# Kernel optimization log

Measured on AMD Instinct MI355X. Metric: run time of the kernel, lower is better.

The kernel has to match this reference:

```python
import jax, jax.numpy as jnp
import numpy as np
from jax import lax


def setup_inputs() -> dict:
    key = jax.random.key(0)
    k1, k2 = jax.random.split(key)
    C, H, W = 64, 224, 224
    C_out, hf, wf = 128, 3, 3
    x = jax.random.normal(k1, (C, H, W), dtype=jnp.float32)
    kernels = jax.random.normal(k2, (C_out, C, hf, wf), dtype=jnp.float32)
    return {"x": x, "kernels": kernels}


def reference(x, kernels):
    # Original builds im2col columns per output pixel then does k_col @ x_col,
    # i.e. a cross-correlation with 'valid' padding and stride 1.
    # lax.conv_general_dilated computes exactly this (no kernel flip).
    stride = 1
    out = lax.conv_general_dilated(
        x[None],                       # (1, C, H, W) NCHW
        kernels,                       # (C_out, C_in, hf, wf) OIHW
        window_strides=(stride, stride),
        padding="VALID",
        dimension_numbers=("NCHW", "OIHW", "NCHW"),
    )
    return out[0]                      # (C_out, H_out, W_out)
```

## Files before the change

### kernel.cpp

```cpp
#include <hip/hip_runtime.h>
#include <hip/hip_bf16.h>


#define H_IN   224
#define W_IN   224
#define C_OUT  128
#define H_OUT  222
#define W_OUT  222
#define XP     226
#define CPAD   72
#define TW     68

typedef __attribute__((ext_vector_type(8)))  short bf16x8;
typedef __attribute__((ext_vector_type(16))) float f32x16;

static __device__ __forceinline__ unsigned short f2bs(float f) {
    union { __hip_bfloat16 h; unsigned short u; } cv;
    cv.h = __float2bfloat16(f);
    return cv.u;
}

__global__ __launch_bounds__(256)
void transform_w_kernel(const float* __restrict__ w, __hip_bfloat16* __restrict__ wt)
{
    int idx = blockIdx.x * 256 + threadIdx.x;
    if (idx < 9 * 128 * 64) {
        int ij  = idx >> 13;
        int rem = idx & 8191;
        int co  = rem >> 6;
        int c   = rem & 63;
        wt[idx] = __float2bfloat16(w[(co * 64 + c) * 9 + ij]);
    }
}

__global__ __launch_bounds__(256)
void transpose_x_kernel(const float* __restrict__ x, __hip_bfloat16* __restrict__ xt)
{
    __shared__ __align__(16) unsigned short tile[64 * TW];
    const int h  = blockIdx.y;
    const int w0 = blockIdx.x * 64;
    const int t  = threadIdx.x;

    {
        const int wq = (t & 15) * 4;
        const int c0 = t >> 4;
        #pragma unroll
        for (int p = 0; p < 4; ++p) {
            const int c  = c0 + p * 16;
            const int wg = w0 + wq;
            float4 v = make_float4(0.f, 0.f, 0.f, 0.f);
            if (h < H_IN && wg < W_IN)
                v = *(const float4*)(x + ((size_t)c * H_IN + h) * W_IN + wg);
            ushort4 b;
            b.x = f2bs(v.x); b.y = f2bs(v.y); b.z = f2bs(v.z); b.w = f2bs(v.w);
            *(ushort4*)(tile + c * TW + wq) = b;
        }
    }
    __syncthreads();

    {
        const int wl = t >> 2;
        const int cq = (t & 3) * 16;
        const int wg = w0 + wl;
        if (wg < XP) {
            alignas(16) unsigned short r[16];
            #pragma unroll
            for (int k = 0; k < 16; ++k)
                r[k] = tile[(cq + k) * TW + wl];
            float4* d = (float4*)((unsigned short*)xt + ((size_t)h * XP + wg) * 64 + cq);
            d[0] = ((const float4*)r)[0];
            d[1] = ((const float4*)r)[1];
        }
    }
}

__global__ __launch_bounds__(256)
void conv_mfma_kernel(const __hip_bfloat16* __restrict__ xt,
                      const __hip_bfloat16* __restrict__ wt,
                      float* __restrict__ out)
{
    __shared__ __hip_bfloat16 xs[10 * 34 * CPAD];
    const int ow0 = blockIdx.x * 32;
    const int oh0 = blockIdx.y * 8;
    const int co0 = blockIdx.z * 64;
    const int tid = threadIdx.x;

    for (int q = tid; q < 10 * 34 * 8; q += 256) {
        int sub = q & 7;
        int pix = q >> 3;
        int row = pix / 34;
        int wc  = pix - row * 34;
        *(float4*)(xs + (row * 34 + wc) * CPAD + sub * 8) =
            *(const float4*)(xt + ((oh0 + row) * XP + (ow0 + wc)) * 64 + sub * 8);
    }
    __syncthreads();

    const int wave = tid >> 6;
    const int lane = tid & 63;
    const int n    = lane & 31;
    const int h    = lane >> 5;

    f32x16 acc[2][2] = {};

    #pragma unroll
    for (int i = 0; i < 3; ++i) {
        bf16x8 afr[3][2][4];
        #pragma unroll
        for (int jj = 0; jj < 3; ++jj)
            #pragma unroll
            for (int mi = 0; mi < 2; ++mi)
                #pragma unroll
                for (int t = 0; t < 4; ++t)
                    afr[jj][mi][t] = *(const bf16x8*)(wt +
                        ((i * 3 + jj) * 128 + co0 + mi * 32 + n) * 64 + t * 16 + h * 8);

        #pragma unroll
        for (int jj = 0; jj < 3; ++jj) {
            #pragma unroll
            for (int t = 0; t < 4; ++t) {
                bf16x8 bfr[2];
                #pragma unroll
                for (int ni = 0; ni < 2; ++ni)
                    bfr[ni] = *(const bf16x8*)(xs +
                        ((wave * 2 + ni + i) * 34 + n + jj) * CPAD + t * 16 + h * 8);
                #pragma unroll
                for (int mi = 0; mi < 2; ++mi)
                    #pragma unroll
                    for (int ni = 0; ni < 2; ++ni)
                        acc[mi][ni] = __builtin_amdgcn_mfma_f32_32x32x16_bf16(
                            afr[jj][mi][t], bfr[ni], acc[mi][ni], 0, 0, 0);
            }
        }
    }

    #pragma unroll
    for (int mi = 0; mi < 2; ++mi) {
        #pragma unroll
        for (int ni = 0; ni < 2; ++ni) {
            const int oh = oh0 + wave * 2 + ni;
            const int ow = ow0 + n;
            if (oh < H_OUT && ow < W_OUT) {
                #pragma unroll
                for (int r = 0; r < 16; ++r) {
                    int co = co0 + mi * 32 + (r & 3) + 8 * (r >> 2) + 4 * h;
                    out[(size_t)co * (H_OUT * W_OUT) + oh * W_OUT + ow] = acc[mi][ni][r];
                }
            }
        }
    }
}

extern "C" void kernel_launch(void* const* d_in, const int* in_sizes, int n_in,
                              void* d_out, int out_size, void* d_ws, size_t ws_size,
                              hipStream_t stream)
{
    const float* x = (const float*)d_in[0];
    const float* w = (const float*)d_in[1];
    float* out     = (float*)d_out;

    __hip_bfloat16* xt = (__hip_bfloat16*)d_ws;
    __hip_bfloat16* wt = (__hip_bfloat16*)((char*)d_ws + (size_t)XP * XP * 64 * 2);

    transform_w_kernel<<<288, 256, 0, stream>>>(w, wt);
    transpose_x_kernel<<<dim3(4, XP), 256, 0, stream>>>(x, xt);
    conv_mfma_kernel<<<dim3(7, 28, 2), 256, 0, stream>>>(xt, wt, out);
}
```

Measured before the change: 98.14 us.

## Stage weights through double-buffered LDS with a blocked weight layout

```diff
diff --git a/kernel.cpp b/kernel.cpp
--- a/kernel.cpp
+++ b/kernel.cpp
@@ -29,7 +29,8 @@
         int rem = idx & 8191;
         int co  = rem >> 6;
         int c   = rem & 63;
-        wt[idx] = __float2bfloat16(w[(co * 64 + c) * 9 + ij]);
+        wt[((ij * 8 + (c >> 3)) * 128 + co) * 8 + (c & 7)] =
+            __float2bfloat16(w[(co * 64 + c) * 9 + ij]);
     }
 }
 
@@ -80,6 +81,7 @@
                       float* __restrict__ out)
 {
     __shared__ __hip_bfloat16 xs[10 * 34 * CPAD];
+    __shared__ __hip_bfloat16 wsb[2][8 * 64 * 8];
     const int ow0 = blockIdx.x * 32;
     const int oh0 = blockIdx.y * 8;
     const int co0 = blockIdx.z * 64;
@@ -93,51 +95,77 @@
         *(float4*)(xs + (row * 34 + wc) * CPAD + sub * 8) =
             *(const float4*)(xt + ((oh0 + row) * XP + (ow0 + wc)) * 64 + sub * 8);
     }
+    {
+        const float4* s = (const float4*)(wt + (size_t)co0 * 8);
+        #pragma unroll
+        for (int k = 0; k < 2; ++k) {
+            int q  = k * 256 + tid;
+            int ks = q >> 6;
+            int cc = q & 63;
+            *(float4*)(&wsb[0][(ks * 64 + cc) * 8]) =
+                *(const float4*)(wt + ((0 * 8 + ks) * 128 + co0 + cc) * 8);
+        }
+        (void)s;
+    }
     __syncthreads();
 
     const int wave = tid >> 6;
     const int lane = tid & 63;
     const int n    = lane & 31;
     const int h    = lane >> 5;
+    const int r0   = wave * 2;
 
     f32x16 acc[2][2] = {};
 
     #pragma unroll
-    for (int i = 0; i < 3; ++i) {
-        bf16x8 afr[3][2][4];
+    for (int p = 0; p < 9; ++p) {
+        const int i  = p / 3;
+        const int jj = p - i * 3;
+        const int cb = p & 1;
+
+        float4 pf[2];
+        int ks0 = 0, cc0 = 0, ks1 = 0, cc1 = 0;
+        if (p < 8) {
+            #pragma unroll
+            for (int k = 0; k < 2; ++k) {
+                int q  = k * 256 + tid;
+                int ks = q >> 6;
+                int cc = q & 63;
+                pf[k] = *(const float4*)(wt + (((p + 1) * 8 + ks) * 128 + co0 + cc) * 8);
+                if (k == 0) { ks0 = ks; cc0 = cc; } else { ks1 = ks; cc1 = cc; }
+            }
+        }
+
         #pragma unroll
-        for (int jj = 0; jj < 3; ++jj)
+        for (int t = 0; t < 4; ++t) {
+            bf16x8 afr[2], bfr[2];
+            #pragma unroll
+            for (int mi = 0; mi < 2; ++mi)
+                afr[mi] = *(const bf16x8*)(&wsb[cb][((t * 2 + h) * 64 + mi * 32 + n) * 8]);
+            #pragma unroll
+            for (int ni = 0; ni < 2; ++ni)
+                bfr[ni] = *(const bf16x8*)(xs +
+                    ((i + r0 + ni) * 34 + n + jj) * CPAD + t * 16 + h * 8);
             #pragma unroll
             for (int mi = 0; mi < 2; ++mi)
                 #pragma unroll
-                for (int t = 0; t < 4; ++t)
-                    afr[jj][mi][t] = *(const bf16x8*)(wt +
-                        ((i * 3 + jj) * 128 + co0 + mi * 32 + n) * 64 + t * 16 + h * 8);
+                for (int ni = 0; ni < 2; ++ni)
+                    acc[mi][ni] = __builtin_amdgcn_mfma_f32_32x32x16_bf16(
+                        afr[mi], bfr[ni], acc[mi][ni], 0, 0, 0);
+        }
 
-        #pragma unroll
-        for (int jj = 0; jj < 3; ++jj) {
-            #pragma unroll
-            for (int t = 0; t < 4; ++t) {
-                bf16x8 bfr[2];
-                #pragma unroll
-                for (int ni = 0; ni < 2; ++ni)
-                    bfr[ni] = *(const bf16x8*)(xs +
-                        ((wave * 2 + ni + i) * 34 + n + jj) * CPAD + t * 16 + h * 8);
-                #pragma unroll
-                for (int mi = 0; mi < 2; ++mi)
-                    #pragma unroll
-                    for (int ni = 0; ni < 2; ++ni)
-                        acc[mi][ni] = __builtin_amdgcn_mfma_f32_32x32x16_bf16(
-                            afr[jj][mi][t], bfr[ni], acc[mi][ni], 0, 0, 0);
-            }
+        if (p < 8) {
+            *(float4*)(&wsb[1 - cb][(ks0 * 64 + cc0) * 8]) = pf[0];
+            *(float4*)(&wsb[1 - cb][(ks1 * 64 + cc1) * 8]) = pf[1];
         }
+        __syncthreads();
     }
 
     #pragma unroll
     for (int mi = 0; mi < 2; ++mi) {
         #pragma unroll
         for (int ni = 0; ni < 2; ++ni) {
-            const int oh = oh0 + wave * 2 + ni;
+            const int oh = oh0 + r0 + ni;
             const int ow = ow0 + n;
             if (oh < H_OUT && ow < W_OUT) {
                 #pragma unroll
```

New measurement: 88.08 us. 10.3% less time.

## Swizzle LDS input tile and reorder weight layout for coalesced fragment loads

Applied to the files above, without the earlier changes.

```diff
diff --git a/kernel.cpp b/kernel.cpp
--- a/kernel.cpp
+++ b/kernel.cpp
@@ -8,7 +8,6 @@
 #define H_OUT  222
 #define W_OUT  222
 #define XP     226
-#define CPAD   72
 #define TW     68
 
 typedef __attribute__((ext_vector_type(8)))  short bf16x8;
@@ -29,7 +28,8 @@
         int rem = idx & 8191;
         int co  = rem >> 6;
         int c   = rem & 63;
-        wt[idx] = __float2bfloat16(w[(co * 64 + c) * 9 + ij]);
+        wt[((ij * 8 + (c >> 3)) * 128 + co) * 8 + (c & 7)] =
+            __float2bfloat16(w[(co * 64 + c) * 9 + ij]);
     }
 }
 
@@ -79,7 +79,7 @@
                       const __hip_bfloat16* __restrict__ wt,
                       float* __restrict__ out)
 {
-    __shared__ __hip_bfloat16 xs[10 * 34 * CPAD];
+    __shared__ __hip_bfloat16 xs[10 * 34 * 64];
     const int ow0 = blockIdx.x * 32;
     const int oh0 = blockIdx.y * 8;
     const int co0 = blockIdx.z * 64;
@@ -90,7 +90,8 @@
         int pix = q >> 3;
         int row = pix / 34;
         int wc  = pix - row * 34;
-        *(float4*)(xs + (row * 34 + wc) * CPAD + sub * 8) =
+        int chunk = sub ^ (wc & 3);
+        *(float4*)(xs + pix * 64 + chunk * 8) =
             *(const float4*)(xt + ((oh0 + row) * XP + (ow0 + wc)) * 64 + sub * 8);
     }
     __syncthreads();
@@ -99,37 +100,39 @@
     const int lane = tid & 63;
     const int n    = lane & 31;
     const int h    = lane >> 5;
+    const int r0   = wave * 2;
 
     f32x16 acc[2][2] = {};
 
     #pragma unroll
-    for (int i = 0; i < 3; ++i) {
-        bf16x8 afr[3][2][4];
+    for (int p = 0; p < 9; ++p) {
+        const int i  = p / 3;
+        const int jj = p - i * 3;
+
+        bf16x8 afr[4][2];
         #pragma unroll
-        for (int jj = 0; jj < 3; ++jj)
+        for (int t = 0; t < 4; ++t)
+            #pragma unroll
+            for (int mi = 0; mi < 2; ++mi)
+                afr[t][mi] = *(const bf16x8*)(wt +
+                    ((p * 8 + t * 2 + h) * 128 + co0 + mi * 32 + n) * 8);
+
+        #pragma unroll
+        for (int t = 0; t < 4; ++t) {
+            bf16x8 bfr[2];
+            #pragma unroll
+            for (int ni = 0; ni < 2; ++ni) {
+                const int wc    = n + jj;
+                const int pix   = (i + r0 + ni) * 34 + wc;
+                const int chunk = (t * 2 + h) ^ (wc & 3);
+                bfr[ni] = *(const bf16x8*)(xs + pix * 64 + chunk * 8);
+            }
             #pragma unroll
             for (int mi = 0; mi < 2; ++mi)
                 #pragma unroll
-                for (int t = 0; t < 4; ++t)
-                    afr[jj][mi][t] = *(const bf16x8*)(wt +
-                        ((i * 3 + jj) * 128 + co0 + mi * 32 + n) * 64 + t * 16 + h * 8);
-
-        #pragma unroll
-        for (int jj = 0; jj < 3; ++jj) {
-            #pragma unroll
-            for (int t = 0; t < 4; ++t) {
-                bf16x8 bfr[2];
-                #pragma unroll
                 for (int ni = 0; ni < 2; ++ni)
-                    bfr[ni] = *(const bf16x8*)(xs +
-                        ((wave * 2 + ni + i) * 34 + n + jj) * CPAD + t * 16 + h * 8);
-                #pragma unroll
-                for (int mi = 0; mi < 2; ++mi)
-                    #pragma unroll
-                    for (int ni = 0; ni < 2; ++ni)
-                        acc[mi][ni] = __builtin_amdgcn_mfma_f32_32x32x16_bf16(
-                            afr[jj][mi][t], bfr[ni], acc[mi][ni], 0, 0, 0);
-            }
+                    acc[mi][ni] = __builtin_amdgcn_mfma_f32_32x32x16_bf16(
+                        afr[t][mi], bfr[ni], acc[mi][ni], 0, 0, 0);
         }
     }
 
@@ -137,7 +140,7 @@
     for (int mi = 0; mi < 2; ++mi) {
         #pragma unroll
         for (int ni = 0; ni < 2; ++ni) {
-            const int oh = oh0 + wave * 2 + ni;
+            const int oh = oh0 + r0 + ni;
             const int ow = ow0 + n;
             if (oh < H_OUT && ow < W_OUT) {
                 #pragma unroll
```

New measurement: 91.93 us. 6.3% less time.
